# Optimization experiments

Hardware: AMD Instinct MI355X
Metric: run time of the kernel (lower is better)

Reference implementation:

```python
import jax, jax.numpy as jnp
import numpy as np

C = 256          # channels
H = 8            # attn_heads
B = 2048         # number of graphs
NPG = 128        # nodes per graph
N = B * NPG      # total nodes
EPS = 1e-5


def setup_inputs() -> dict:
    key = jax.random.key(0)
    ks = jax.random.split(key, 16)
    s = 1.0 / np.sqrt(C)
    seg = jnp.repeat(jnp.arange(B, dtype=jnp.int32), NPG)          # sorted, all segments present
    batch = jnp.stack([seg, seg], axis=1)                           # [N, 2]; column 0 = graph id
    return {
        "x": jax.random.normal(ks[0], (N, C), dtype=jnp.float32),
        "batch": batch,
        "num_graphs": B,
        "W1": jax.random.normal(ks[1], (C, C), dtype=jnp.float32) * s,
        "b1": jnp.zeros((C,), jnp.float32),
        "gamma": jnp.ones((C,), jnp.float32),
        "beta": jnp.zeros((C,), jnp.float32),
        "W2": jax.random.normal(ks[2], (C, C), dtype=jnp.float32) * s,
        "b2": jnp.zeros((C,), jnp.float32),
        "Wq": jax.random.normal(ks[3], (C, C), dtype=jnp.float32) * s,
        "bq": jnp.zeros((C,), jnp.float32),
        "Wk": jax.random.normal(ks[4], (C, C), dtype=jnp.float32) * s,
        "bk": jnp.zeros((C,), jnp.float32),
        "Wv": jax.random.normal(ks[5], (C, C), dtype=jnp.float32) * s,
        "bv": jnp.zeros((C,), jnp.float32),
        "Wo": jax.random.normal(ks[6], (C, C), dtype=jnp.float32) * s,
        "bo": jnp.zeros((C,), jnp.float32),
        "Wr": jax.random.normal(ks[7], (1, C), dtype=jnp.float32) * s,
        "br": jnp.zeros((1,), jnp.float32),
    }


def reference(x, batch, num_graphs, W1, b1, gamma, beta, W2, b2,
              Wq, bq, Wk, bk, Wv, bv, Wo, bo, Wr, br):
    seg = batch[:, 0]                                   # [N] graph ids, sorted
    Dh = C // H
    scale = 1.0 / np.sqrt(Dh)

    # trunk: Linear -> BatchNorm1d (train-mode batch stats) -> ReLU -> Linear
    h = x @ W1.T + b1                                   # [N, C]
    mu = h.mean(axis=0)
    var = h.var(axis=0)                                 # biased, as torch uses for normalization
    h = (h - mu) * jax.lax.rsqrt(var + EPS) * gamma + beta
    h = jax.nn.relu(h)
    h = h @ W2.T + b2                                   # [N, C]

    # single-query MHA pooled per graph segment (query = ones(C))
    q = jnp.ones((C,), h.dtype)
    qh = (q @ Wq.T + bq).reshape(H, Dh)                 # [H, Dh] shared across graphs
    kh = (h @ Wk.T + bk).reshape(N, H, Dh)              # [N, H, Dh]
    vh = (h @ Wv.T + bv).reshape(N, H, Dh)

    logits = jnp.einsum('nhd,hd->nh', kh, qh) * scale   # [N, H]
    # segment softmax over each graph's nodes
    m = jax.ops.segment_max(logits, seg, num_segments=num_graphs)   # [B, H]
    p = jnp.exp(logits - m[seg])                                     # [N, H]
    denom = jax.ops.segment_sum(p, seg, num_segments=num_graphs)     # [B, H]
    attn = p / denom[seg]                                            # [N, H]

    pooled = jax.ops.segment_sum(attn[:, :, None] * vh, seg,
                                 num_segments=num_graphs)            # [B, H, Dh]
    pooled = pooled.reshape(num_graphs, C) @ Wo.T + bo               # out_proj -> [B, C]

    out = jnp.tanh(pooled @ Wr.T + br)                               # [B, 1]
    return out
```

## Files before the change

### kernel.cpp

```cpp
#include <hip/hip_runtime.h>
#include <hip/hip_bf16.h>
#include <math.h>

#define C_DIM 256
#define H_HEADS 8
#define B_GRAPHS 2048
#define NPG 128
#define N_NODES (B_GRAPHS * NPG)
#define EPS 1e-5f
#define SCALE_ATT 0.17677669529663687f

typedef short bf16x8 __attribute__((ext_vector_type(8)));
typedef float f32x4 __attribute__((ext_vector_type(4)));

__device__ __forceinline__ unsigned short f2bf(float f) {
    __hip_bfloat16 h = __float2bfloat16(f);
    union { __hip_bfloat16 h; unsigned short u; } cv; cv.h = h; return cv.u;
}
__device__ __forceinline__ float bf2f(unsigned short u) {
    union { unsigned int i; float f; } v; v.i = ((unsigned int)u) << 16; return v.f;
}

__global__ __launch_bounds__(256) void prepA_kernel(
    const float* __restrict__ W1, unsigned short* __restrict__ W1bf,
    const float* __restrict__ Wq, const float* __restrict__ bq,
    const float* __restrict__ Wk, const float* __restrict__ Wo,
    const float* __restrict__ Wr,
    float* __restrict__ wk_eff, float* __restrict__ wor)
{
    __shared__ float qhS[256];
    __shared__ float WrS[256];
    const int t = threadIdx.x;
    if (blockIdx.x < 256) {
        int i = blockIdx.x * 256 + t;
        W1bf[i] = f2bf(W1[i]);
        return;
    }
    {
        float s = bq[t];
        const float* row = Wq + (size_t)t * 256;
        for (int c = 0; c < 256; c += 4) {
            float4 v = *(const float4*)&row[c];
            s += v.x + v.y + v.z + v.w;
        }
        qhS[t] = s;
        WrS[t] = Wr[t];
    }
    __syncthreads();
    for (int head = 0; head < 8; ++head) {
        float acc = 0.f;
        #pragma unroll 4
        for (int d = 0; d < 32; ++d)
            acc = fmaf(Wk[(size_t)(head * 32 + d) * 256 + t], qhS[head * 32 + d], acc);
        wk_eff[head * 256 + t] = acc * SCALE_ATT;
    }
    {
        float acc = 0.f;
        for (int j2 = 0; j2 < 256; ++j2)
            acc = fmaf(Wo[(size_t)j2 * 256 + t], WrS[j2], acc);
        wor[t] = acc;
    }
}

__global__ __launch_bounds__(256) void gemm_kernel(
    const float* __restrict__ x, const unsigned short* __restrict__ W1bf,
    unsigned short* __restrict__ h1,
    float* __restrict__ psum, float* __restrict__ psum2,
    const float* __restrict__ W2, const float* __restrict__ Wv,
    const float* __restrict__ wk_eff, const float* __restrict__ wor,
    const float* __restrict__ b2, const float* __restrict__ bv,
    const float* __restrict__ bo, const float* __restrict__ Wr,
    const float* __restrict__ br,
    unsigned short* __restrict__ WBg, float* __restrict__ c0)
{
    __shared__ unsigned short Wlds[256 * 40];
    __shared__ unsigned short Xlds[128 * 40];
    __shared__ float red1[256], red2[256];
    __shared__ float worS[32];
    const int t = threadIdx.x;

    if (blockIdx.x >= 2048) {
        const int head = blockIdx.x - 2048;
        float* wkS = red1;
        float* vS  = red2;
        wkS[t] = wk_eff[head * 256 + t];
        if (t < 32) worS[t] = wor[head * 32 + t];
        __syncthreads();
        float acc = 0.f;
        #pragma unroll 4
        for (int cp = 0; cp < 256; ++cp)
            acc = fmaf(W2[(size_t)cp * 256 + t], wkS[cp], acc);
        WBg[head * 256 + t] = f2bf(acc);
        float accv = 0.f;
        #pragma unroll 4
        for (int d = 0; d < 32; ++d)
            accv = fmaf(Wv[(size_t)(head * 32 + d) * 256 + t], worS[d], accv);
        vS[t] = accv;
        __syncthreads();
        float accg = 0.f;
        #pragma unroll 4
        for (int cp = 0; cp < 256; ++cp)
            accg = fmaf(W2[(size_t)cp * 256 + t], vS[cp], accg);
        WBg[(8 + head) * 256 + t] = f2bf(accg);
        float part = b2[t] * accv;
        if (head == 0) {
            part += bv[t] * wor[t] + bo[t] * Wr[t];
            if (t == 0) part += br[0];
        }
        #pragma unroll
        for (int s = 1; s < 64; s <<= 1) part += __shfl_xor(part, s);
        if ((t & 63) == 0) atomicAdd(c0, part);
        return;
    }

    const int lane = t & 63, w = t >> 6;
    const int l15 = lane & 15, kg = lane >> 4;
    const size_t n0 = (size_t)blockIdx.x * 128;

    red1[t] = 0.f;
    red2[t] = 0.f;

    f32x4 acc0[16], acc1[16];
    #pragma unroll
    for (int mt = 0; mt < 16; ++mt) {
        acc0[mt] = (f32x4){0.f, 0.f, 0.f, 0.f};
        acc1[mt] = (f32x4){0.f, 0.f, 0.f, 0.f};
    }

    for (int kk = 0; kk < 8; ++kk) {
        if (kk) __syncthreads();
        #pragma unroll
        for (int p = 0; p < 4; ++p) {
            int i = p * 256 + t;
            {
                int row = i >> 3, kq = i & 7;
                float4 v = *(const float4*)&x[(n0 + row) * 256 + kk * 32 + kq * 4];
                ushort4 u;
                u.x = f2bf(v.x); u.y = f2bf(v.y); u.z = f2bf(v.z); u.w = f2bf(v.w);
                *(ushort4*)&Xlds[row * 40 + kq * 4] = u;
            }
            {
                int row = i >> 2, seg = i & 3;
                bf16x8 bv8 = *(const bf16x8*)&W1bf[(size_t)row * 256 + kk * 32 + seg * 8];
                *(bf16x8*)&Wlds[row * 40 + seg * 8] = bv8;
            }
        }
        __syncthreads();
        bf16x8 b0 = *(const bf16x8*)&Xlds[(w * 32 + l15) * 40 + kg * 8];
        bf16x8 b1 = *(const bf16x8*)&Xlds[(w * 32 + 16 + l15) * 40 + kg * 8];
        #pragma unroll
        for (int mt = 0; mt < 16; ++mt) {
            bf16x8 a = *(const bf16x8*)&Wlds[(mt * 16 + l15) * 40 + kg * 8];
            acc0[mt] = __builtin_amdgcn_mfma_f32_16x16x32_bf16(a, b0, acc0[mt], 0, 0, 0);
            acc1[mt] = __builtin_amdgcn_mfma_f32_16x16x32_bf16(a, b1, acc1[mt], 0, 0, 0);
        }
    }

    const size_t rb0 = (n0 + w * 32 + l15) * 256;
    const size_t rb1 = rb0 + 16 * 256;
    #pragma unroll
    for (int mt = 0; mt < 16; ++mt) {
        f32x4 a0 = acc0[mt], a1 = acc1[mt];
        ushort4 u0, u1;
        u0.x = f2bf(a0[0]); u0.y = f2bf(a0[1]); u0.z = f2bf(a0[2]); u0.w = f2bf(a0[3]);
        u1.x = f2bf(a1[0]); u1.y = f2bf(a1[1]); u1.z = f2bf(a1[2]); u1.w = f2bf(a1[3]);
        *(ushort4*)&h1[rb0 + mt * 16 + kg * 4] = u0;
        *(ushort4*)&h1[rb1 + mt * 16 + kg * 4] = u1;
        float s1v[4], s2v[4];
        #pragma unroll
        for (int r = 0; r < 4; ++r) {
            s1v[r] = a0[r] + a1[r];
            s2v[r] = a0[r] * a0[r] + a1[r] * a1[r];
        }
        #pragma unroll
        for (int r = 0; r < 4; ++r) {
            #pragma unroll
            for (int s = 1; s < 16; s <<= 1) {
                s1v[r] += __shfl_xor(s1v[r], s);
                s2v[r] += __shfl_xor(s2v[r], s);
            }
        }
        if (l15 == 0) {
            #pragma unroll
            for (int r = 0; r < 4; ++r) {
                atomicAdd(&red1[mt * 16 + kg * 4 + r], s1v[r]);
                atomicAdd(&red2[mt * 16 + kg * 4 + r], s2v[r]);
            }
        }
    }
    __syncthreads();
    atomicAdd(&psum[t], red1[t]);
    atomicAdd(&psum2[t], red2[t]);
}

__global__ __launch_bounds__(256) void fused_kernel(
    const unsigned short* __restrict__ h1,
    const float* __restrict__ psum, const float* __restrict__ psum2,
    const float* __restrict__ gamma, const float* __restrict__ beta,
    const unsigned short* __restrict__ WBg,
    const float* __restrict__ c0_g, float* __restrict__ out)
{
    __shared__ float scS[256], shS[256];
    __shared__ float LG[128 * 17];
    __shared__ float redH[8];

    const int t = threadIdx.x;
    const int g = blockIdx.x;
    const int lane = t & 63, w = t >> 6;
    const int l15 = lane & 15, kg = lane >> 4;

    {
        const float invN = 1.0f / (float)N_NODES;
        float S = psum[t], S2 = psum2[t];
        float mu = S * invN;
        float var = S2 * invN - mu * mu;
        float rstd = rsqrtf(var + EPS);
        float gmr = gamma[t] * rstd;
        scS[t] = gmr;
        shS[t] = beta[t] - mu * gmr;
    }
    bf16x8 af[8];
    #pragma unroll
    for (int kt = 0; kt < 8; ++kt)
        af[kt] = *(const bf16x8*)&WBg[l15 * 256 + kt * 32 + kg * 8];
    __syncthreads();

    const size_t base0 = ((size_t)g * 128 + w * 32 + l15) * 256;
    const size_t base1 = base0 + 16 * 256;
    f32x4 acc0 = {0.f, 0.f, 0.f, 0.f}, acc1 = {0.f, 0.f, 0.f, 0.f};
    #pragma unroll
    for (int kt = 0; kt < 8; ++kt) {
        const int cc = kt * 32 + kg * 8;
        bf16x8 h0 = *(const bf16x8*)&h1[base0 + cc];
        bf16x8 h1v = *(const bf16x8*)&h1[base1 + cc];
        f32x4 scA = *(const f32x4*)&scS[cc];
        f32x4 scB = *(const f32x4*)&scS[cc + 4];
        f32x4 shA = *(const f32x4*)&shS[cc];
        f32x4 shB = *(const f32x4*)&shS[cc + 4];
        bf16x8 b0, b1;
        #pragma unroll
        for (int e = 0; e < 4; ++e) {
            b0[e]     = (short)f2bf(fmaxf(fmaf(bf2f((unsigned short)h0[e]),      scA[e], shA[e]), 0.f));
            b0[e + 4] = (short)f2bf(fmaxf(fmaf(bf2f((unsigned short)h0[e + 4]),  scB[e], shB[e]), 0.f));
            b1[e]     = (short)f2bf(fmaxf(fmaf(bf2f((unsigned short)h1v[e]),     scA[e], shA[e]), 0.f));
            b1[e + 4] = (short)f2bf(fmaxf(fmaf(bf2f((unsigned short)h1v[e + 4]), scB[e], shB[e]), 0.f));
        }
        acc0 = __builtin_amdgcn_mfma_f32_16x16x32_bf16(af[kt], b0, acc0, 0, 0, 0);
        acc1 = __builtin_amdgcn_mfma_f32_16x16x32_bf16(af[kt], b1, acc1, 0, 0, 0);
    }
    #pragma unroll
    for (int r = 0; r < 4; ++r) {
        LG[(w * 32 + l15) * 17 + kg * 4 + r]      = acc0[r];
        LG[(w * 32 + 16 + l15) * 17 + kg * 4 + r] = acc1[r];
    }
    __syncthreads();

    {
        const int h = t >> 5, j = t & 31;
        float l[4], gv[4];
        #pragma unroll
        for (int q = 0; q < 4; ++q) {
            int n = j + q * 32;
            l[q]  = LG[n * 17 + h];
            gv[q] = LG[n * 17 + 8 + h];
        }
        float m = fmaxf(fmaxf(l[0], l[1]), fmaxf(l[2], l[3]));
        for (int s = 16; s > 0; s >>= 1) m = fmaxf(m, __shfl_xor(m, s, 32));
        float sp = 0.f, sg = 0.f;
        #pragma unroll
        for (int q = 0; q < 4; ++q) {
            float p = expf(l[q] - m);
            sp += p;
            sg = fmaf(p, gv[q], sg);
        }
        for (int s = 16; s > 0; s >>= 1) {
            sp += __shfl_xor(sp, s, 32);
            sg += __shfl_xor(sg, s, 32);
        }
        if (j == 0) redH[h] = sg / sp;
    }
    __syncthreads();
    if (t == 0) {
        float r = c0_g[0];
        #pragma unroll
        for (int h = 0; h < 8; ++h) r += redH[h];
        out[g] = tanhf(r);
    }
}

extern "C" void kernel_launch(void* const* d_in, const int* in_sizes, int n_in,
                              void* d_out, int out_size, void* d_ws, size_t ws_size,
                              hipStream_t stream)
{
    (void)in_sizes; (void)n_in; (void)out_size; (void)ws_size;
    const float* x     = (const float*)d_in[0];
    const float* W1    = (const float*)d_in[3];
    const float* gamma = (const float*)d_in[5];
    const float* beta  = (const float*)d_in[6];
    const float* W2    = (const float*)d_in[7];
    const float* b2    = (const float*)d_in[8];
    const float* Wq    = (const float*)d_in[9];
    const float* bq    = (const float*)d_in[10];
    const float* Wk    = (const float*)d_in[11];
    const float* Wv    = (const float*)d_in[13];
    const float* bv    = (const float*)d_in[14];
    const float* Wo    = (const float*)d_in[15];
    const float* bo    = (const float*)d_in[16];
    const float* Wr    = (const float*)d_in[17];
    const float* br    = (const float*)d_in[18];

    unsigned short* h1   = (unsigned short*)d_ws;
    unsigned short* W1bf = h1 + (size_t)N_NODES * 256;
    unsigned short* WBg  = W1bf + 65536;
    float* fbase = (float*)(WBg + 4096);

    float* wk_eff = fbase;
    float* wor    = fbase + 2048;
    float* psum   = fbase + 2304;
    float* psum2  = fbase + 2560;
    float* c0     = fbase + 2816;

    hipMemsetAsync((void*)psum, 0, 513 * sizeof(float), stream);

    hipLaunchKernelGGL(prepA_kernel, dim3(257), dim3(256), 0, stream,
                       W1, W1bf, Wq, bq, Wk, Wo, Wr, wk_eff, wor);
    hipLaunchKernelGGL(gemm_kernel, dim3(2056), dim3(256), 0, stream,
                       x, W1bf, h1, psum, psum2,
                       W2, Wv, wk_eff, wor, b2, bv, bo, Wr, br, WBg, c0);
    hipLaunchKernelGGL(fused_kernel, dim3(B_GRAPHS), dim3(256), 0, stream,
                       h1, psum, psum2, gamma, beta, WBg, c0, (float*)d_out);
}
```

Measured before the change: 597.9 us.

## Drop prep kernel, fold weight folding into GEMM, use LDS-free register GEMM

```diff
diff --git a/kernel.cpp b/kernel.cpp
--- a/kernel.cpp
+++ b/kernel.cpp
@@ -9,6 +9,7 @@
 #define N_NODES (B_GRAPHS * NPG)
 #define EPS 1e-5f
 #define SCALE_ATT 0.17677669529663687f
+#define GEMM_BLOCKS 4096
 
 typedef short bf16x8 __attribute__((ext_vector_type(8)));
 typedef float f32x4 __attribute__((ext_vector_type(4)));
@@ -21,90 +22,85 @@
     union { unsigned int i; float f; } v; v.i = ((unsigned int)u) << 16; return v.f;
 }
 
-__global__ __launch_bounds__(256) void prepA_kernel(
-    const float* __restrict__ W1, unsigned short* __restrict__ W1bf,
-    const float* __restrict__ Wq, const float* __restrict__ bq,
-    const float* __restrict__ Wk, const float* __restrict__ Wo,
-    const float* __restrict__ Wr,
-    float* __restrict__ wk_eff, float* __restrict__ wor)
-{
-    __shared__ float qhS[256];
-    __shared__ float WrS[256];
-    const int t = threadIdx.x;
-    if (blockIdx.x < 256) {
-        int i = blockIdx.x * 256 + t;
-        W1bf[i] = f2bf(W1[i]);
-        return;
-    }
-    {
-        float s = bq[t];
-        const float* row = Wq + (size_t)t * 256;
-        for (int c = 0; c < 256; c += 4) {
-            float4 v = *(const float4*)&row[c];
-            s += v.x + v.y + v.z + v.w;
-        }
-        qhS[t] = s;
-        WrS[t] = Wr[t];
-    }
-    __syncthreads();
-    for (int head = 0; head < 8; ++head) {
-        float acc = 0.f;
-        #pragma unroll 4
-        for (int d = 0; d < 32; ++d)
-            acc = fmaf(Wk[(size_t)(head * 32 + d) * 256 + t], qhS[head * 32 + d], acc);
-        wk_eff[head * 256 + t] = acc * SCALE_ATT;
-    }
-    {
-        float acc = 0.f;
-        for (int j2 = 0; j2 < 256; ++j2)
-            acc = fmaf(Wo[(size_t)j2 * 256 + t], WrS[j2], acc);
-        wor[t] = acc;
-    }
-}
-
-__global__ __launch_bounds__(256) void gemm_kernel(
-    const float* __restrict__ x, const unsigned short* __restrict__ W1bf,
+__global__ __launch_bounds__(256, 3) void gemm_kernel(
+    const float* __restrict__ x, const float* __restrict__ W1,
     unsigned short* __restrict__ h1,
     float* __restrict__ psum, float* __restrict__ psum2,
     const float* __restrict__ W2, const float* __restrict__ Wv,
-    const float* __restrict__ wk_eff, const float* __restrict__ wor,
     const float* __restrict__ b2, const float* __restrict__ bv,
-    const float* __restrict__ bo, const float* __restrict__ Wr,
-    const float* __restrict__ br,
+    const float* __restrict__ bo,
+    const float* __restrict__ Wq, const float* __restrict__ bq,
+    const float* __restrict__ Wk, const float* __restrict__ Wo,
+    const float* __restrict__ Wr, const float* __restrict__ br,
     unsigned short* __restrict__ WBg, float* __restrict__ c0)
 {
-    __shared__ unsigned short Wlds[256 * 40];
-    __shared__ unsigned short Xlds[128 * 40];
-    __shared__ float red1[256], red2[256];
-    __shared__ float worS[32];
     const int t = threadIdx.x;
 
-    if (blockIdx.x >= 2048) {
-        const int head = blockIdx.x - 2048;
-        float* wkS = red1;
-        float* vS  = red2;
-        wkS[t] = wk_eff[head * 256 + t];
-        if (t < 32) worS[t] = wor[head * 32 + t];
+    if (blockIdx.x >= GEMM_BLOCKS) {
+        __shared__ float qhS[256];
+        __shared__ float wkS[256];
+        __shared__ float vS[256];
+        __shared__ float worP[8][32];
+        __shared__ float worS[32];
+        const int head = blockIdx.x - GEMM_BLOCKS;
+        {
+            float s = bq[t];
+            const float* row = Wq + (size_t)t * 256;
+            for (int c = 0; c < 256; c += 4) {
+                float4 v = *(const float4*)&row[c];
+                s += v.x + v.y + v.z + v.w;
+            }
+            qhS[t] = s;
+        }
+        {
+            int jj = t & 31, grp = t >> 5;
+            float acc = 0.f;
+            #pragma unroll 4
+            for (int m = 0; m < 32; ++m) {
+                int j2 = grp * 32 + m;
+                acc = fmaf(Wo[(size_t)j2 * 256 + head * 32 + jj], Wr[j2], acc);
+            }
+            worP[grp][jj] = acc;
+        }
         __syncthreads();
-        float acc = 0.f;
-        #pragma unroll 4
-        for (int cp = 0; cp < 256; ++cp)
-            acc = fmaf(W2[(size_t)cp * 256 + t], wkS[cp], acc);
-        WBg[head * 256 + t] = f2bf(acc);
+        if (t < 32) {
+            float s = 0.f;
+            #pragma unroll
+            for (int g2 = 0; g2 < 8; ++g2) s += worP[g2][t];
+            worS[t] = s;
+        }
+        {
+            float acc = 0.f;
+            #pragma unroll 4
+            for (int d = 0; d < 32; ++d)
+                acc = fmaf(Wk[(size_t)(head * 32 + d) * 256 + t], qhS[head * 32 + d], acc);
+            wkS[t] = acc * SCALE_ATT;
+        }
+        __syncthreads();
+        {
+            float acc = 0.f;
+            #pragma unroll 4
+            for (int cp = 0; cp < 256; ++cp)
+                acc = fmaf(W2[(size_t)cp * 256 + t], wkS[cp], acc);
+            WBg[head * 256 + t] = f2bf(acc);
+        }
         float accv = 0.f;
         #pragma unroll 4
         for (int d = 0; d < 32; ++d)
             accv = fmaf(Wv[(size_t)(head * 32 + d) * 256 + t], worS[d], accv);
         vS[t] = accv;
         __syncthreads();
-        float accg = 0.f;
-        #pragma unroll 4
-        for (int cp = 0; cp < 256; ++cp)
-            accg = fmaf(W2[(size_t)cp * 256 + t], vS[cp], accg);
-        WBg[(8 + head) * 256 + t] = f2bf(accg);
+        {
+            float acc = 0.f;
+            #pragma unroll 4
+            for (int cp = 0; cp < 256; ++cp)
+                acc = fmaf(W2[(size_t)cp * 256 + t], vS[cp], acc);
+            WBg[(8 + head) * 256 + t] = f2bf(acc);
+        }
         float part = b2[t] * accv;
+        if (t < 32) part += bv[head * 32 + t] * worS[t];
         if (head == 0) {
-            part += bv[t] * wor[t] + bo[t] * Wr[t];
+            part += bo[t] * Wr[t];
             if (t == 0) part += br[0];
         }
         #pragma unroll
@@ -115,82 +111,89 @@
 
     const int lane = t & 63, w = t >> 6;
     const int l15 = lane & 15, kg = lane >> 4;
-    const size_t n0 = (size_t)blockIdx.x * 128;
-
-    red1[t] = 0.f;
-    red2[t] = 0.f;
-
-    f32x4 acc0[16], acc1[16];
-    #pragma unroll
-    for (int mt = 0; mt < 16; ++mt) {
-        acc0[mt] = (f32x4){0.f, 0.f, 0.f, 0.f};
-        acc1[mt] = (f32x4){0.f, 0.f, 0.f, 0.f};
-    }
-
+    const size_t n0 = (size_t)blockIdx.x * 64;
+    const int wc = w * 64;
+
+    f32x4 acc[4][4];
+    #pragma unroll
+    for (int mti = 0; mti < 4; ++mti)
+        #pragma unroll
+        for (int nst = 0; nst < 4; ++nst)
+            acc[mti][nst] = (f32x4){0.f, 0.f, 0.f, 0.f};
+
+    #pragma unroll 2
     for (int kk = 0; kk < 8; ++kk) {
-        if (kk) __syncthreads();
-        #pragma unroll
-        for (int p = 0; p < 4; ++p) {
-            int i = p * 256 + t;
-            {
-                int row = i >> 3, kq = i & 7;
-                float4 v = *(const float4*)&x[(n0 + row) * 256 + kk * 32 + kq * 4];
-                ushort4 u;
-                u.x = f2bf(v.x); u.y = f2bf(v.y); u.z = f2bf(v.z); u.w = f2bf(v.w);
-                *(ushort4*)&Xlds[row * 40 + kq * 4] = u;
-            }
-            {
-                int row = i >> 2, seg = i & 3;
-                bf16x8 bv8 = *(const bf16x8*)&W1bf[(size_t)row * 256 + kk * 32 + seg * 8];
-                *(bf16x8*)&Wlds[row * 40 + seg * 8] = bv8;
-            }
-        }
-        __syncthreads();
-        bf16x8 b0 = *(const bf16x8*)&Xlds[(w * 32 + l15) * 40 + kg * 8];
-        bf16x8 b1 = *(const bf16x8*)&Xlds[(w * 32 + 16 + l15) * 40 + kg * 8];
-        #pragma unroll
-        for (int mt = 0; mt < 16; ++mt) {
-            bf16x8 a = *(const bf16x8*)&Wlds[(mt * 16 + l15) * 40 + kg * 8];
-            acc0[mt] = __builtin_amdgcn_mfma_f32_16x16x32_bf16(a, b0, acc0[mt], 0, 0, 0);
-            acc1[mt] = __builtin_amdgcn_mfma_f32_16x16x32_bf16(a, b1, acc1[mt], 0, 0, 0);
-        }
-    }
-
-    const size_t rb0 = (n0 + w * 32 + l15) * 256;
-    const size_t rb1 = rb0 + 16 * 256;
-    #pragma unroll
-    for (int mt = 0; mt < 16; ++mt) {
-        f32x4 a0 = acc0[mt], a1 = acc1[mt];
-        ushort4 u0, u1;
-        u0.x = f2bf(a0[0]); u0.y = f2bf(a0[1]); u0.z = f2bf(a0[2]); u0.w = f2bf(a0[3]);
-        u1.x = f2bf(a1[0]); u1.y = f2bf(a1[1]); u1.z = f2bf(a1[2]); u1.w = f2bf(a1[3]);
-        *(ushort4*)&h1[rb0 + mt * 16 + kg * 4] = u0;
-        *(ushort4*)&h1[rb1 + mt * 16 + kg * 4] = u1;
-        float s1v[4], s2v[4];
+        const int ko = kk * 32 + kg * 8;
+        bf16x8 af[4];
+        #pragma unroll
+        for (int mti = 0; mti < 4; ++mti) {
+            const float* wp = &W1[(size_t)(wc + mti * 16 + l15) * 256 + ko];
+            float4 w0 = *(const float4*)wp;
+            float4 w1 = *(const float4*)(wp + 4);
+            bf16x8 a;
+            a[0] = (short)f2bf(w0.x); a[1] = (short)f2bf(w0.y);
+            a[2] = (short)f2bf(w0.z); a[3] = (short)f2bf(w0.w);
+            a[4] = (short)f2bf(w1.x); a[5] = (short)f2bf(w1.y);
+            a[6] = (short)f2bf(w1.z); a[7] = (short)f2bf(w1.w);
+            af[mti] = a;
+        }
+        #pragma unroll
+        for (int nst = 0; nst < 4; ++nst) {
+            const float* xp = &x[(n0 + nst * 16 + l15) * 256 + ko];
+            float4 x0 = *(const float4*)xp;
+            float4 x1 = *(const float4*)(xp + 4);
+            bf16x8 b;
+            b[0] = (short)f2bf(x0.x); b[1] = (short)f2bf(x0.y);
+            b[2] = (short)f2bf(x0.z); b[3] = (short)f2bf(x0.w);
+            b[4] = (short)f2bf(x1.x); b[5] = (short)f2bf(x1.y);
+            b[6] = (short)f2bf(x1.z); b[7] = (short)f2bf(x1.w);
+            #pragma unroll
+            for (int mti = 0; mti < 4; ++mti)
+                acc[mti][nst] = __builtin_amdgcn_mfma_f32_16x16x32_bf16(af[mti], b, acc[mti][nst], 0, 0, 0);
+        }
+    }
+
+    #pragma unroll
+    for (int nst = 0; nst < 4; ++nst) {
+        const size_t rowb = (n0 + nst * 16 + l15) * 256 + wc + kg * 4;
+        #pragma unroll
+        for (int mti = 0; mti < 4; ++mti) {
+            f32x4 a = acc[mti][nst];
+            ushort4 u;
+            u.x = f2bf(a[0]); u.y = f2bf(a[1]); u.z = f2bf(a[2]); u.w = f2bf(a[3]);
+            *(ushort4*)&h1[rowb + mti * 16] = u;
+        }
+    }
+
+    float s1[4][4], s2[4][4];
+    #pragma unroll
+    for (int mti = 0; mti < 4; ++mti)
         #pragma unroll
         for (int r = 0; r < 4; ++r) {
-            s1v[r] = a0[r] + a1[r];
-            s2v[r] = a0[r] * a0[r] + a1[r] * a1[r];
-        }
-        #pragma unroll
-        for (int r = 0; r < 4; ++r) {
-            #pragma unroll
-            for (int s = 1; s < 16; s <<= 1) {
-                s1v[r] += __shfl_xor(s1v[r], s);
-                s2v[r] += __shfl_xor(s2v[r], s);
-            }
-        }
-        if (l15 == 0) {
+            float a0 = acc[mti][0][r], a1 = acc[mti][1][r];
+            float a2 = acc[mti][2][r], a3 = acc[mti][3][r];
+            s1[mti][r] = (a0 + a1) + (a2 + a3);
+            s2[mti][r] = (a0 * a0 + a1 * a1) + (a2 * a2 + a3 * a3);
+        }
+    #pragma unroll
+    for (int s = 1; s < 16; s <<= 1)
+        #pragma unroll
+        for (int mti = 0; mti < 4; ++mti)
             #pragma unroll
             for (int r = 0; r < 4; ++r) {
-                atomicAdd(&red1[mt * 16 + kg * 4 + r], s1v[r]);
-                atomicAdd(&red2[mt * 16 + kg * 4 + r], s2v[r]);
+                s1[mti][r] += __shfl_xor(s1[mti][r], s);
+                s2[mti][r] += __shfl_xor(s2[mti][r], s);
             }
-        }
-    }
-    __syncthreads();
-    atomicAdd(&psum[t], red1[t]);
-    atomicAdd(&psum2[t], red2[t]);
+    if (l15 == 0) {
+        #pragma unroll
+        for (int mti = 0; mti < 4; ++mti)
+            #pragma unroll
+            for (int r = 0; r < 4; ++r) {
+                int c = wc + mti * 16 + kg * 4 + r;
+                atomicAdd(&psum[c], s1[mti][r]);
+                atomicAdd(&psum2[c], s2[mti][r]);
+            }
+    }
 }
 
 __global__ __launch_bounds__(256) void fused_kernel(
@@ -309,24 +312,19 @@
     const float* Wr    = (const float*)d_in[17];
     const float* br    = (const float*)d_in[18];
 
-    unsigned short* h1   = (unsigned short*)d_ws;
-    unsigned short* W1bf = h1 + (size_t)N_NODES * 256;
-    unsigned short* WBg  = W1bf + 65536;
+    unsigned short* h1  = (unsigned short*)d_ws;
+    unsigned short* WBg = h1 + (size_t)N_NODES * 256;
     float* fbase = (float*)(WBg + 4096);
 
-    float* wk_eff = fbase;
-    float* wor    = fbase + 2048;
-    float* psum   = fbase + 2304;
-    float* psum2  = fbase + 2560;
-    float* c0     = fbase + 2816;
+    float* psum  = fbase;
+    float* psum2 = fbase + 256;
+    float* c0    = fbase + 512;
 
     hipMemsetAsync((void*)psum, 0, 513 * sizeof(float), stream);
 
-    hipLaunchKernelGGL(prepA_kernel, dim3(257), dim3(256), 0, stream,
-                       W1, W1bf, Wq, bq, Wk, Wo, Wr, wk_eff, wor);
-    hipLaunchKernelGGL(gemm_kernel, dim3(2056), dim3(256), 0, stream,
-                       x, W1bf, h1, psum, psum2,
-                       W2, Wv, wk_eff, wor, b2, bv, bo, Wr, br, WBg, c0);
+    hipLaunchKernelGGL(gemm_kernel, dim3(GEMM_BLOCKS + 8), dim3(256), 0, stream,
+                       x, W1, h1, psum, psum2,
+                       W2, Wv, b2, bv, bo, Wq, bq, Wk, Wo, Wr, br, WBg, c0);
     hipLaunchKernelGGL(fused_kernel, dim3(B_GRAPHS), dim3(256), 0, stream,
                        h1, psum, psum2, gamma, beta, WBg, c0, (float*)d_out);
 }
```

Result: slower. 875.5 us (+46.4%).
